# Optimization experiments

Measured on AMD Instinct MI355X. Metric: run time of the kernel, lower is better.

The kernel has to match this reference:

```python
import jax, jax.numpy as jnp
import numpy as np

DIM = 512
NUM_HEADS = 16
WIN = (7, 7)
N = WIN[0] * WIN[1]          # 49 tokens per window
NW = 64                      # windows per image
B = 32                       # images
B_ = B * NW                  # total windows = 2048
SCALE = (DIM // NUM_HEADS) ** -0.5


def _relative_position_index(wh, ww):
    coords = np.stack(np.meshgrid(np.arange(wh), np.arange(ww), indexing='ij'))  # (2, wh, ww)
    coords = coords.reshape(2, -1)                                               # (2, N)
    rel = coords[:, :, None] - coords[:, None, :]                                # (2, N, N)
    rel = rel.transpose(1, 2, 0).astype(np.int32)                                # (N, N, 2)
    rel[:, :, 0] += wh - 1
    rel[:, :, 1] += ww - 1
    rel[:, :, 0] *= 2 * ww - 1
    return jnp.asarray(rel.sum(-1), dtype=jnp.int32)                             # (N, N)


def _shift_mask(nw, n):
    # Swin-style additive mask: 0 within groups, -100 across groups.
    rng = np.random.RandomState(0)
    groups = rng.randint(0, 4, size=(nw, n)).astype(np.int32)
    m = np.where(groups[:, :, None] == groups[:, None, :], 0.0, -100.0)
    return jnp.asarray(m, dtype=jnp.float32)                                     # (nW, N, N)


def setup_inputs() -> dict:
    key = jax.random.key(0)
    ks = jax.random.split(key, 5)
    x = jax.random.normal(ks[0], (B_, N, DIM), dtype=jnp.float32)
    qkv_w = jax.random.normal(ks[1], (3 * DIM, DIM), dtype=jnp.float32) * 0.02
    qkv_b = jnp.zeros((3 * DIM,), dtype=jnp.float32)
    proj_w = jax.random.normal(ks[2], (DIM, DIM), dtype=jnp.float32) * 0.02
    proj_b = jnp.zeros((DIM,), dtype=jnp.float32)
    rpb_table = jax.random.normal(ks[3], ((2 * WIN[0] - 1) * (2 * WIN[1] - 1), NUM_HEADS), dtype=jnp.float32) * 0.02
    mask = _shift_mask(NW, N)
    rel_idx = _relative_position_index(*WIN)
    return {"x": x, "mask": mask, "qkv_w": qkv_w, "qkv_b": qkv_b,
            "proj_w": proj_w, "proj_b": proj_b, "rpb_table": rpb_table,
            "rel_idx": rel_idx}


def reference(x, mask, qkv_w, qkv_b, proj_w, proj_b, rpb_table, rel_idx):
    b_, n, c = x.shape
    nh = rpb_table.shape[1]
    d = c // nh
    # qkv projection: (B_, N, 3, nH, d) -> q, k, v each (B_, nH, N, d)
    qkv = (jnp.einsum('bnc,oc->bno', x, qkv_w) + qkv_b).reshape(b_, n, 3, nh, d)
    qkv = jnp.transpose(qkv, (2, 0, 3, 1, 4))
    q, k, v = qkv[0], qkv[1], qkv[2]
    attn = jnp.einsum('bhnd,bhmd->bhnm', q * SCALE, k)                     # (B_, nH, N, N)
    # gathered relative position bias: (N*N, nH) -> (nH, N, N)
    bias = rpb_table[rel_idx.reshape(-1)].reshape(n, n, nh)
    attn = attn + jnp.transpose(bias, (2, 0, 1))[None]
    # shifted-window mask add
    nw = mask.shape[0]
    attn = attn.reshape(b_ // nw, nw, nh, n, n) + mask[None, :, None]
    attn = attn.reshape(b_, nh, n, n)
    attn = jax.nn.softmax(attn, axis=-1)
    out = jnp.einsum('bhnm,bhmd->bhnd', attn, v)                           # (B_, nH, N, d)
    out = jnp.transpose(out, (0, 2, 1, 3)).reshape(b_, n, c)
    return jnp.einsum('bnc,oc->bno', out, proj_w) + proj_b
```

## Files before the change

kernel.cpp:

```cpp
#include <hip/hip_runtime.h>
#include <hip/hip_bf16.h>
#include <stdint.h>
#include <stddef.h>

#define B_TOT   2048
#define NTOK    49
#define CDIM    512
#define NHEAD   16
#define HD      32
#define NWIN    64
#define MROWS   (B_TOT*NTOK)
#define O_QKV   1536
#define SCALE_F 0.17677669529663687f

typedef short bf16x8 __attribute__((ext_vector_type(8)));
typedef float f32x4  __attribute__((ext_vector_type(4)));

__device__ __forceinline__ unsigned short f2bf(float f){
  union { float f; unsigned u; } v; v.f = f;
  unsigned r = v.u + 0x7fffu + ((v.u >> 16) & 1u);
  return (unsigned short)(r >> 16);
}

#define GL16(g,l) __builtin_amdgcn_global_load_lds( \
      (const __attribute__((address_space(1))) unsigned int*)(g), \
      (__attribute__((address_space(3))) unsigned int*)(l), 16, 0, 0)

__global__ void k_cvt_x(const float* __restrict__ x, unsigned short* __restrict__ xb, int n4){
  int i = blockIdx.x * blockDim.x + threadIdx.x;
  int st = gridDim.x * blockDim.x;
  for (; i < n4; i += st){
    float4 v = ((const float4*)x)[i];
    uint2 o;
    o.x = (unsigned)f2bf(v.x) | ((unsigned)f2bf(v.y) << 16);
    o.y = (unsigned)f2bf(v.z) | ((unsigned)f2bf(v.w) << 16);
    ((uint2*)xb)[i] = o;
  }
}

__global__ void k_prep(const float* __restrict__ qkv_w, const float* __restrict__ proj_w,
                       const float* __restrict__ rpb, const int* __restrict__ rel_idx,
                       const float* __restrict__ mask,
                       unsigned short* __restrict__ wqkv, unsigned short* __restrict__ wproj,
                       float* __restrict__ bmb){
  int i = blockIdx.x * blockDim.x + threadIdx.x;
  int st = gridDim.x * blockDim.x;
  for (int j = i; j < O_QKV*CDIM; j += st) wqkv[j] = f2bf(qkv_w[j]);
  for (int j = i; j < CDIM*CDIM;  j += st) wproj[j] = f2bf(proj_w[j]);
  const int TOT = NWIN * NHEAD * NTOK * NTOK;
  for (int j = i; j < TOT; j += st){
    int wi = j / (NHEAD * NTOK * NTOK);
    int t  = j - wi * (NHEAD * NTOK * NTOK);
    int h  = t / (NTOK * NTOK);
    int rc = t - h * (NTOK * NTOK);
    bmb[j] = mask[wi * (NTOK*NTOK) + rc] + rpb[rel_idx[rc] * NHEAD + h];
  }
}


#define LDA_(P,RG,MI,S) (*(const bf16x8*)(rA + (P)*32768 + (RG)*16384 + (MI)*2048 + ((S)?(cb0^64):cb0)))
#define LDB_(P,CG,NI,S) (*(const bf16x8*)(rB + (P)*32768 + (CG)*16384 + (NI)*2048 + ((S)?(cb0^64):cb0)))

#define STAGE_A(P,HG,KT) { \
    GL16(aS0 + (size_t)(HG)*64*Kb + (size_t)(KT)*128, ldA + (P)*32768 + (HG)*16384); \
    GL16(aS1 + (size_t)(HG)*64*Kb + (size_t)(KT)*128, ldA + (P)*32768 + (HG)*16384 + 8192); }
#define STAGE_B(P,HG,KT) { \
    GL16(bS0 + (size_t)(HG)*32*Kb + (size_t)(KT)*128, ldB + (P)*32768 + (HG)*16384); \
    GL16(bS1 + (size_t)(HG)*32*Kb + (size_t)(KT)*128, ldB + (P)*32768 + (HG)*16384 + 8192); }

#define PHASE(P,RG,CG,DOA,DOB,VM,...) { \
  if (DOA){ _Pragma("unroll") for (int mi=0;mi<4;++mi){ af[mi][0]=LDA_(P,RG,mi,0); af[mi][1]=LDA_(P,RG,mi,1);} } \
  if (DOB){ _Pragma("unroll") for (int ni=0;ni<2;++ni){ bf_[ni][0]=LDB_(P,CG,ni,0); bf_[ni][1]=LDB_(P,CG,ni,1);} } \
  __VA_ARGS__; \
  __builtin_amdgcn_s_barrier(); \
  asm volatile("s_waitcnt lgkmcnt(0)" ::: "memory"); \
  __builtin_amdgcn_sched_barrier(0); \
  __builtin_amdgcn_s_setprio(1); \
  _Pragma("unroll") for (int s=0;s<2;++s) \
    _Pragma("unroll") for (int mi=0;mi<4;++mi) \
      _Pragma("unroll") for (int ni=0;ni<2;++ni) \
        acc[(RG)*4+mi][(CG)*2+ni] = __builtin_amdgcn_mfma_f32_16x16x32_bf16(af[mi][s], bf_[ni][s], acc[(RG)*4+mi][(CG)*2+ni], 0,0,0); \
  __builtin_amdgcn_s_setprio(0); \
  if (VM) asm volatile("s_waitcnt vmcnt(4)" ::: "memory"); \
  __builtin_amdgcn_s_barrier(); \
  asm volatile("" ::: "memory"); \
}

template<int OUT_F32>
__global__ __launch_bounds__(512, 2) void k_gemm8(const unsigned short* __restrict__ Ag,
                                                  const unsigned short* __restrict__ Bg,
                                                  const float* __restrict__ bias,
                                                  void* __restrict__ Cout,
                                                  int Ndim, int Kdim){
  extern __shared__ char smem[];
  const int tid = threadIdx.x;
  const int wv = tid >> 6, lane = tid & 63, lg = lane >> 4, lr = lane & 15;
  const int wm = wv >> 2, wn = wv & 3;

  const int nbx = gridDim.x;
  const int nwg = nbx * gridDim.y;
  const int id  = blockIdx.y * nbx + blockIdx.x;
  const int nid = (id & 7) * (nwg >> 3) + (id >> 3);
  const int bx = nid % nbx, by = nid / nbx;
  const int bm0 = by * 256, bn0 = bx * 256;
  const size_t Kb = (size_t)Kdim * 2;
  const int NIT = Kdim >> 7;

  const int srow = tid >> 3;
  const int scb  = ((tid & 7) << 4) ^ ((srow & 7) << 4);
  const char* aS0 = (const char*)Ag + (size_t)(bm0 + srow) * Kb + scb;
  const char* aS1 = (const char*)Ag + (size_t)(bm0 + 128 + srow) * Kb + scb;
  const char* bS0 = (const char*)Bg + (size_t)(bn0 + (srow>>5)*64 + (srow&31)) * Kb + scb;
  const char* bS1 = (const char*)Bg + (size_t)(bn0 + 128 + (srow>>5)*64 + (srow&31)) * Kb + scb;
  char* ldA = smem + wv * 1024;
  char* ldB = smem + 65536 + wv * 1024;

  const int cb0 = (lg * 16) ^ ((lr & 7) << 4);
  const char* rA = smem + (wm*64 + lr) * 128;
  const char* rB = smem + 65536 + (wn*32 + lr) * 128;

  f32x4 acc[8][4];
  #pragma unroll
  for (int i = 0; i < 8; ++i)
    #pragma unroll
    for (int j = 0; j < 4; ++j)
      #pragma unroll
      for (int r = 0; r < 4; ++r) acc[i][j][r] = 0.f;

  bf16x8 af[4][2], bf_[2][2];

  STAGE_A(0,0,0); STAGE_A(0,1,0); STAGE_B(0,0,0); STAGE_B(0,1,0);
  STAGE_A(1,0,1); STAGE_B(1,1,1);
  asm volatile("s_waitcnt vmcnt(4)" ::: "memory");
  __builtin_amdgcn_s_barrier();
  asm volatile("" ::: "memory");

  for (int it = 0; it < NIT; ++it){
    const int T = 2*it;
    PHASE(0, 0,0, 1,1, 0, STAGE_A(1,1,(T+1)))
    PHASE(0, 0,1, 0,1, 0, STAGE_B(1,0,(T+1)))
    PHASE(0, 1,1, 1,0, 0, STAGE_A(0,0,(T+2)))
    PHASE(0, 1,0, 0,1, 1, STAGE_B(0,1,(T+2)))
    PHASE(1, 0,0, 1,1, 0, STAGE_A(0,1,(T+2)))
    PHASE(1, 0,1, 0,1, 0, STAGE_B(0,0,(T+2)))
    PHASE(1, 1,1, 1,0, 0, STAGE_A(1,0,(T+3)))
    PHASE(1, 1,0, 0,1, 1, STAGE_B(1,1,(T+3)))
  }

  #pragma unroll
  for (int RG = 0; RG < 2; ++RG)
    #pragma unroll
    for (int mi = 0; mi < 4; ++mi)
      #pragma unroll
      for (int CG = 0; CG < 2; ++CG)
        #pragma unroll
        for (int ni = 0; ni < 2; ++ni){
          f32x4 v = acc[RG*4+mi][CG*2+ni];
          const int col = bn0 + wn*64 + CG*32 + ni*16 + lr;
          const float bc = bias[col];
          #pragma unroll
          for (int r = 0; r < 4; ++r){
            const int row = bm0 + wm*128 + RG*64 + mi*16 + lg*4 + r;
            const float t = v[r] + bc;
            if (OUT_F32) ((float*)Cout)[(size_t)row * Ndim + col] = t;
            else ((unsigned short*)Cout)[(size_t)row * Ndim + col] = f2bf(t);
          }
        }
}

__global__ __launch_bounds__(256) void k_attn(const unsigned short* __restrict__ qkv,
                                              const float* __restrict__ bm,
                                              unsigned short* __restrict__ ao){
  __shared__ unsigned short P[4][64*64];
  const int wv = threadIdx.x >> 6, lane = threadIdx.x & 63;
  const int lg = lane >> 4, lr = lane & 15;
  const int gw = blockIdx.x * 4 + wv;
  const int w = gw >> 4, h = gw & 15, wi = w & (NWIN - 1);

  bf16x8 zf; f32x4 z4;
  #pragma unroll
  for (int j = 0; j < 8; ++j) zf[j] = 0;
  #pragma unroll
  for (int j = 0; j < 4; ++j) z4[j] = 0.f;

  const unsigned short* qb = qkv + (size_t)w * NTOK * O_QKV + h * HD;

  bf16x8 qf[4], kf[4];
  #pragma unroll
  for (int mi = 0; mi < 4; ++mi){
    int t = mi*16 + lr;
    qf[mi] = (t < NTOK) ? *(const bf16x8*)(qb + (size_t)t * O_QKV + lg*8) : zf;
    kf[mi] = (t < NTOK) ? *(const bf16x8*)(qb + 512 + (size_t)t * O_QKV + lg*8) : zf;
  }
  f32x4 s[4][4];
  #pragma unroll
  for (int mi = 0; mi < 4; ++mi)
    #pragma unroll
    for (int ni = 0; ni < 4; ++ni)
      s[mi][ni] = __builtin_amdgcn_mfma_f32_16x16x32_bf16(qf[mi], kf[ni], z4, 0, 0, 0);

  const float* bmp = bm + (size_t)(wi * NHEAD + h) * (NTOK * NTOK);
  float rs[4][4];
  #pragma unroll
  for (int mi = 0; mi < 4; ++mi){
    #pragma unroll
    for (int r = 0; r < 4; ++r){
      int row = mi*16 + lg*4 + r;
      float v[4];
      #pragma unroll
      for (int ni = 0; ni < 4; ++ni){
        int col = ni*16 + lr;
        float t = s[mi][ni][r] * SCALE_F;
        if (row < NTOK && col < NTOK) t += bmp[row * NTOK + col];
        if (col >= NTOK) t = -1e30f;
        v[ni] = t;
      }
      float mx = fmaxf(fmaxf(v[0], v[1]), fmaxf(v[2], v[3]));
      mx = fmaxf(mx, __shfl_xor(mx, 1));
      mx = fmaxf(mx, __shfl_xor(mx, 2));
      mx = fmaxf(mx, __shfl_xor(mx, 4));
      mx = fmaxf(mx, __shfl_xor(mx, 8));
      float sum = 0.f;
      #pragma unroll
      for (int ni = 0; ni < 4; ++ni){
        float p = __expf(v[ni] - mx);
        sum += p;
        s[mi][ni][r] = p;
      }
      sum += __shfl_xor(sum, 1);
      sum += __shfl_xor(sum, 2);
      sum += __shfl_xor(sum, 4);
      sum += __shfl_xor(sum, 8);
      rs[mi][r] = sum;
    }
  }

  char* Pb = (char*)P[wv];
  #pragma unroll
  for (int mi = 0; mi < 4; ++mi)
    #pragma unroll
    for (int ni = 0; ni < 4; ++ni)
      #pragma unroll
      for (int r = 0; r < 4; ++r){
        int row = mi*16 + lg*4 + r, col = ni*16 + lr;
        int byte = (row << 7) + (col << 1);
        byte ^= (row & 7) << 4;
        *(unsigned short*)(Pb + byte) = f2bf(s[mi][ni][r]);
      }

  const unsigned short* vb = qkv + (size_t)w * NTOK * O_QKV + 1024 + h * HD;
  f32x4 o[4][2];
  #pragma unroll
  for (int mi = 0; mi < 4; ++mi)
    #pragma unroll
    for (int ni = 0; ni < 2; ++ni)
      #pragma unroll
      for (int r = 0; r < 4; ++r) o[mi][ni][r] = 0.f;

  #pragma unroll
  for (int ss = 0; ss < 2; ++ss){
    bf16x8 vf[2];
    #pragma unroll
    for (int ni = 0; ni < 2; ++ni)
      #pragma unroll
      for (int j = 0; j < 8; ++j){
        int t = ss*32 + lg*8 + j;
        vf[ni][j] = (t < NTOK) ? (short)vb[(size_t)t * O_QKV + ni*16 + lr] : (short)0;
      }
    #pragma unroll
    for (int mi = 0; mi < 4; ++mi){
      int row = mi*16 + lr;
      int byte = (row << 7) + ((ss*64 + lg*16) ^ ((row & 7) << 4));
      bf16x8 pf = *(const bf16x8*)(Pb + byte);
      #pragma unroll
      for (int ni = 0; ni < 2; ++ni)
        o[mi][ni] = __builtin_amdgcn_mfma_f32_16x16x32_bf16(pf, vf[ni], o[mi][ni], 0, 0, 0);
    }
  }

  unsigned short* aop = ao + (size_t)w * NTOK * CDIM + h * HD;
  #pragma unroll
  for (int mi = 0; mi < 4; ++mi)
    #pragma unroll
    for (int ni = 0; ni < 2; ++ni)
      #pragma unroll
      for (int r = 0; r < 4; ++r){
        int row = mi*16 + lg*4 + r, col = ni*16 + lr;
        if (row < NTOK)
          aop[(size_t)row * CDIM + col] = f2bf(o[mi][ni][r] / rs[mi][r]);
      }
}

extern "C" void kernel_launch(void* const* d_in, const int* in_sizes, int n_in,
                              void* d_out, int out_size, void* d_ws, size_t ws_size,
                              hipStream_t stream){
  const float* x      = (const float*)d_in[0];
  const float* mask   = (const float*)d_in[1];
  const float* qkv_w  = (const float*)d_in[2];
  const float* qkv_b  = (const float*)d_in[3];
  const float* proj_w = (const float*)d_in[4];
  const float* proj_b = (const float*)d_in[5];
  const float* rpb    = (const float*)d_in[6];
  const int*   rel_i  = (const int*)d_in[7];

  char* ws = (char*)d_ws;
  unsigned short* xb    = (unsigned short*)(ws);
  unsigned short* qkvb  = (unsigned short*)(ws + 102760448);
  unsigned short* wqkv  = (unsigned short*)(ws + 411041792);
  unsigned short* wproj = (unsigned short*)(ws + 412614656);
  float*          bmb   = (float*)(ws + 413138944);

  (void)hipFuncSetAttribute(reinterpret_cast<const void*>(&k_gemm8<0>),
                            hipFuncAttributeMaxDynamicSharedMemorySize, 131072);
  (void)hipFuncSetAttribute(reinterpret_cast<const void*>(&k_gemm8<1>),
                            hipFuncAttributeMaxDynamicSharedMemorySize, 131072);

  k_cvt_x<<<2048, 256, 0, stream>>>(x, xb, MROWS * CDIM / 4);
  k_prep<<<512, 256, 0, stream>>>(qkv_w, proj_w, rpb, rel_i, mask, wqkv, wproj, bmb);
  k_gemm8<0><<<dim3(O_QKV/256, MROWS/256), 512, 131072, stream>>>(xb, wqkv, qkv_b, qkvb, O_QKV, CDIM);
  k_attn<<<(B_TOT * NHEAD) / 4, 256, 0, stream>>>(qkvb, bmb, xb);
  k_gemm8<1><<<dim3(CDIM/256, MROWS/256), 512, 131072, stream>>>(xb, wproj, proj_b, d_out, CDIM, CDIM);
}
```

Before: 587.0 us.

## Restructure window attention: transposed scores, padded bias table, vectorized V staging via LDS

The bias+mask table is precomputed padded to 64 key columns, with -1e30 in the padding, so the attention kernel reads it as aligned float4 vectors with no bounds checks. Scores are computed as K·Qᵀ, so each lane holds one query row and the softmax reductions need only two cross-lane shuffles. V is loaded with 16-byte vector loads and transposed into swizzled LDS instead of scalar strided global loads. Softmax normalization is folded into P before the bf16 cast. LDS per wave grows, and the layout of the bias table changes.

After: 505.2 us. 13.9% less time.

```diff
diff --git a/kernel.cpp b/kernel.cpp
--- a/kernel.cpp
+++ b/kernel.cpp
@@ -47,16 +47,20 @@
   int st = gridDim.x * blockDim.x;
   for (int j = i; j < O_QKV*CDIM; j += st) wqkv[j] = f2bf(qkv_w[j]);
   for (int j = i; j < CDIM*CDIM;  j += st) wproj[j] = f2bf(proj_w[j]);
-  const int TOT = NWIN * NHEAD * NTOK * NTOK;
+  const int TOT = NWIN * NHEAD * NTOK * 64;
   for (int j = i; j < TOT; j += st){
-    int wi = j / (NHEAD * NTOK * NTOK);
-    int t  = j - wi * (NHEAD * NTOK * NTOK);
-    int h  = t / (NTOK * NTOK);
-    int rc = t - h * (NTOK * NTOK);
-    bmb[j] = mask[wi * (NTOK*NTOK) + rc] + rpb[rel_idx[rc] * NHEAD + h];
-  }
-}
-
+    int wh  = j / (NTOK*64);
+    int rem = j - wh * (NTOK*64);
+    int qt  = rem >> 6, kt = rem & 63;
+    int wi = wh >> 4, h = wh & 15;
+    float v;
+    if (kt < NTOK){
+      int rc = qt * NTOK + kt;
+      v = mask[wi * (NTOK*NTOK) + rc] + rpb[rel_idx[rc] * NHEAD + h];
+    } else v = -1e30f;
+    bmb[j] = v;
+  }
+}
 
 #define LDA_(P,RG,MI,S) (*(const bf16x8*)(rA + (P)*32768 + (RG)*16384 + (MI)*2048 + ((S)?(cb0^64):cb0)))
 #define LDB_(P,CG,NI,S) (*(const bf16x8*)(rB + (P)*32768 + (CG)*16384 + (NI)*2048 + ((S)?(cb0^64):cb0)))
@@ -171,123 +175,136 @@
 __global__ __launch_bounds__(256) void k_attn(const unsigned short* __restrict__ qkv,
                                               const float* __restrict__ bm,
                                               unsigned short* __restrict__ ao){
-  __shared__ unsigned short P[4][64*64];
+  __shared__ char lds[4][12288];
   const int wv = threadIdx.x >> 6, lane = threadIdx.x & 63;
   const int lg = lane >> 4, lr = lane & 15;
   const int gw = blockIdx.x * 4 + wv;
   const int w = gw >> 4, h = gw & 15, wi = w & (NWIN - 1);
-
-  bf16x8 zf; f32x4 z4;
-  #pragma unroll
-  for (int j = 0; j < 8; ++j) zf[j] = 0;
-  #pragma unroll
-  for (int j = 0; j < 4; ++j) z4[j] = 0.f;
-
-  const unsigned short* qb = qkv + (size_t)w * NTOK * O_QKV + h * HD;
+  char* Vt = lds[wv];
+  char* P  = lds[wv] + 4096;
+
+  const unsigned short* base = qkv + (size_t)w * NTOK * O_QKV + h * HD;
+
+  const int vkt = lane >> 2, vch = lane & 3;
+  bf16x8 vld[4];
+  #pragma unroll
+  for (int t = 0; t < 4; ++t){
+    int kt = 16*t + vkt; int kts = kt < NTOK ? kt : NTOK-1;
+    vld[t] = *(const bf16x8*)(base + 1024 + (size_t)kts * O_QKV + vch * 8);
+  }
 
   bf16x8 qf[4], kf[4];
   #pragma unroll
+  for (int i = 0; i < 4; ++i){
+    int t = 16*i + lr; int ts = t < NTOK ? t : NTOK-1;
+    qf[i] = *(const bf16x8*)(base + (size_t)ts * O_QKV + lg*8);
+    kf[i] = *(const bf16x8*)(base + 512 + (size_t)ts * O_QKV + lg*8);
+  }
+
+  const float* bmp = bm + (size_t)(wi * NHEAD + h) * (NTOK * 64);
+  f32x4 bias[4][4];
+  #pragma unroll
   for (int mi = 0; mi < 4; ++mi){
-    int t = mi*16 + lr;
-    qf[mi] = (t < NTOK) ? *(const bf16x8*)(qb + (size_t)t * O_QKV + lg*8) : zf;
-    kf[mi] = (t < NTOK) ? *(const bf16x8*)(qb + 512 + (size_t)t * O_QKV + lg*8) : zf;
-  }
-  f32x4 s[4][4];
+    int qt = 16*mi + lr; int qtc = qt < NTOK ? qt : NTOK-1;
+    #pragma unroll
+    for (int ni = 0; ni < 4; ++ni)
+      bias[mi][ni] = *(const f32x4*)(bmp + qtc*64 + ni*16 + lg*4);
+  }
+
+  f32x4 z4 = {0.f, 0.f, 0.f, 0.f};
+  f32x4 s2[4][4];
+  #pragma unroll
+  for (int ni = 0; ni < 4; ++ni)
+    #pragma unroll
+    for (int mi = 0; mi < 4; ++mi)
+      s2[ni][mi] = __builtin_amdgcn_mfma_f32_16x16x32_bf16(kf[ni], qf[mi], z4, 0, 0, 0);
+
+  #pragma unroll
+  for (int t = 0; t < 4; ++t){
+    int kt = 16*t + vkt;
+    #pragma unroll
+    for (int j = 0; j < 8; ++j){
+      int d = vch*8 + j;
+      int swz = ((d & 7) ^ (d >> 3)) & 7;
+      int byte = d*128 + ((2*kt) ^ (swz << 4));
+      *(unsigned short*)(Vt + byte) = (unsigned short)vld[t][j];
+    }
+  }
+
+  #pragma unroll
+  for (int mi = 0; mi < 4; ++mi){
+    float v[4][4];
+    float mx = -1e30f;
+    #pragma unroll
+    for (int ni = 0; ni < 4; ++ni)
+      #pragma unroll
+      for (int r = 0; r < 4; ++r){
+        float t = s2[ni][mi][r] * SCALE_F + bias[mi][ni][r];
+        v[ni][r] = t;
+        mx = fmaxf(mx, t);
+      }
+    mx = fmaxf(mx, __shfl_xor(mx, 16));
+    mx = fmaxf(mx, __shfl_xor(mx, 32));
+    float sum = 0.f;
+    #pragma unroll
+    for (int ni = 0; ni < 4; ++ni)
+      #pragma unroll
+      for (int r = 0; r < 4; ++r){
+        float p = __expf(v[ni][r] - mx);
+        v[ni][r] = p;
+        sum += p;
+      }
+    sum += __shfl_xor(sum, 16);
+    sum += __shfl_xor(sum, 32);
+    float rn = 1.0f / sum;
+    const int qt = 16*mi + lr;
+    #pragma unroll
+    for (int ni = 0; ni < 4; ++ni){
+      unsigned p0 = (unsigned)f2bf(v[ni][0]*rn) | ((unsigned)f2bf(v[ni][1]*rn) << 16);
+      unsigned p1 = (unsigned)f2bf(v[ni][2]*rn) | ((unsigned)f2bf(v[ni][3]*rn) << 16);
+      uint2 pw; pw.x = p0; pw.y = p1;
+      int byte = qt*128 + ((32*ni + 8*lg) ^ ((lr & 7) << 4));
+      *(uint2*)(P + byte) = pw;
+    }
+  }
+
+  f32x4 o[4][2];
   #pragma unroll
   for (int mi = 0; mi < 4; ++mi)
     #pragma unroll
-    for (int ni = 0; ni < 4; ++ni)
-      s[mi][ni] = __builtin_amdgcn_mfma_f32_16x16x32_bf16(qf[mi], kf[ni], z4, 0, 0, 0);
-
-  const float* bmp = bm + (size_t)(wi * NHEAD + h) * (NTOK * NTOK);
-  float rs[4][4];
-  #pragma unroll
-  for (int mi = 0; mi < 4; ++mi){
-    #pragma unroll
-    for (int r = 0; r < 4; ++r){
-      int row = mi*16 + lg*4 + r;
-      float v[4];
-      #pragma unroll
-      for (int ni = 0; ni < 4; ++ni){
-        int col = ni*16 + lr;
-        float t = s[mi][ni][r] * SCALE_F;
-        if (row < NTOK && col < NTOK) t += bmp[row * NTOK + col];
-        if (col >= NTOK) t = -1e30f;
-        v[ni] = t;
-      }
-      float mx = fmaxf(fmaxf(v[0], v[1]), fmaxf(v[2], v[3]));
-      mx = fmaxf(mx, __shfl_xor(mx, 1));
-      mx = fmaxf(mx, __shfl_xor(mx, 2));
-      mx = fmaxf(mx, __shfl_xor(mx, 4));
-      mx = fmaxf(mx, __shfl_xor(mx, 8));
-      float sum = 0.f;
-      #pragma unroll
-      for (int ni = 0; ni < 4; ++ni){
-        float p = __expf(v[ni] - mx);
-        sum += p;
-        s[mi][ni][r] = p;
-      }
-      sum += __shfl_xor(sum, 1);
-      sum += __shfl_xor(sum, 2);
-      sum += __shfl_xor(sum, 4);
-      sum += __shfl_xor(sum, 8);
-      rs[mi][r] = sum;
+    for (int ni = 0; ni < 2; ++ni)
+      #pragma unroll
+      for (int r = 0; r < 4; ++r) o[mi][ni][r] = 0.f;
+
+  #pragma unroll
+  for (int s = 0; s < 2; ++s){
+    bf16x8 pf[4], vf[2];
+    #pragma unroll
+    for (int mi = 0; mi < 4; ++mi)
+      pf[mi] = *(const bf16x8*)(P + (16*mi + lr)*128 + ((64*s + 16*lg) ^ ((lr & 7) << 4)));
+    #pragma unroll
+    for (int ni = 0; ni < 2; ++ni){
+      int d = 16*ni + lr;
+      int swz = ((d & 7) ^ (d >> 3)) & 7;
+      vf[ni] = *(const bf16x8*)(Vt + d*128 + ((64*s + 16*lg) ^ (swz << 4)));
     }
-  }
-
-  char* Pb = (char*)P[wv];
+    #pragma unroll
+    for (int mi = 0; mi < 4; ++mi)
+      #pragma unroll
+      for (int ni = 0; ni < 2; ++ni)
+        o[mi][ni] = __builtin_amdgcn_mfma_f32_16x16x32_bf16(pf[mi], vf[ni], o[mi][ni], 0, 0, 0);
+  }
+
+  unsigned short* aop = ao + (size_t)w * NTOK * CDIM + h * HD;
   #pragma unroll
   for (int mi = 0; mi < 4; ++mi)
     #pragma unroll
-    for (int ni = 0; ni < 4; ++ni)
+    for (int ni = 0; ni < 2; ++ni)
       #pragma unroll
       for (int r = 0; r < 4; ++r){
-        int row = mi*16 + lg*4 + r, col = ni*16 + lr;
-        int byte = (row << 7) + (col << 1);
-        byte ^= (row & 7) << 4;
-        *(unsigned short*)(Pb + byte) = f2bf(s[mi][ni][r]);
-      }
-
-  const unsigned short* vb = qkv + (size_t)w * NTOK * O_QKV + 1024 + h * HD;
-  f32x4 o[4][2];
-  #pragma unroll
-  for (int mi = 0; mi < 4; ++mi)
-    #pragma unroll
-    for (int ni = 0; ni < 2; ++ni)
-      #pragma unroll
-      for (int r = 0; r < 4; ++r) o[mi][ni][r] = 0.f;
-
-  #pragma unroll
-  for (int ss = 0; ss < 2; ++ss){
-    bf16x8 vf[2];
-    #pragma unroll
-    for (int ni = 0; ni < 2; ++ni)
-      #pragma unroll
-      for (int j = 0; j < 8; ++j){
-        int t = ss*32 + lg*8 + j;
-        vf[ni][j] = (t < NTOK) ? (short)vb[(size_t)t * O_QKV + ni*16 + lr] : (short)0;
-      }
-    #pragma unroll
-    for (int mi = 0; mi < 4; ++mi){
-      int row = mi*16 + lr;
-      int byte = (row << 7) + ((ss*64 + lg*16) ^ ((row & 7) << 4));
-      bf16x8 pf = *(const bf16x8*)(Pb + byte);
-      #pragma unroll
-      for (int ni = 0; ni < 2; ++ni)
-        o[mi][ni] = __builtin_amdgcn_mfma_f32_16x16x32_bf16(pf, vf[ni], o[mi][ni], 0, 0, 0);
-    }
-  }
-
-  unsigned short* aop = ao + (size_t)w * NTOK * CDIM + h * HD;
-  #pragma unroll
-  for (int mi = 0; mi < 4; ++mi)
-    #pragma unroll
-    for (int ni = 0; ni < 2; ++ni)
-      #pragma unroll
-      for (int r = 0; r < 4; ++r){
-        int row = mi*16 + lg*4 + r, col = ni*16 + lr;
+        int row = 16*mi + 4*lg + r, col = 16*ni + lr;
         if (row < NTOK)
-          aop[(size_t)row * CDIM + col] = f2bf(o[mi][ni][r] / rs[mi][r]);
+          aop[(size_t)row * CDIM + col] = f2bf(o[mi][ni][r]);
       }
 }
 
```
